# Kernel optimization log

Hardware: AMD Instinct MI355X
Metric: run time of the kernel (lower is better)

Reference implementation:

```python
import jax, jax.numpy as jnp
import numpy as np

B, T, D, H = 64, 512, 256, 512

def _xavier(key, shape):
    fan_in, fan_out = shape
    lim = np.sqrt(6.0 / (fan_in + fan_out))
    return jax.random.uniform(key, shape, jnp.float32, -lim, lim)

def setup_inputs() -> dict:
    key = jax.random.key(0)
    ks = jax.random.split(key, 16)
    inp = {
        'x': jax.random.normal(ks[0], (B, T, D), jnp.float32),
        'h': jax.random.normal(ks[1], (B, H), jnp.float32),
        'We2h': _xavier(ks[2], (D, H)),            # err_in2h (no bias)
        'Wr_x': _xavier(ks[3], (D, H)),
        'Wr_h': _xavier(ks[4], (H, H)),
        'Wr_e': _xavier(ks[5], (H, H)),
        'br': jnp.zeros((H,), jnp.float32),
        'Wz_x': _xavier(ks[6], (D, H)),
        'Wz_h': _xavier(ks[7], (H, H)),
        'Wz_e': _xavier(ks[8], (H, H)),
        'bz': jnp.ones((H,), jnp.float32),         # update_bias.fill_(1.0)
        'Wn_x': _xavier(ks[9], (D, H)),
        'Wn_h': _xavier(ks[10], (H, H)),
        'Wn_e': _xavier(ks[11], (H, H)),
        'bn': jnp.zeros((H,), jnp.float32),
        'Wo': _xavier(ks[12], (H, D)),             # readout Linear(H, D)
        'bo': jnp.zeros((D,), jnp.float32),
    }
    return inp

def reference(x, h, We2h, Wr_x, Wr_h, Wr_e, br, Wz_x, Wz_h, Wz_e, bz, Wn_x, Wn_h, Wn_e, bn, Wo, bo):
    # Precompute all input-to-hidden projections in large GEMMs: [B,T,H]
    x_e = jnp.einsum('btd,dh->bth', x, We2h)
    x_r = jnp.einsum('btd,dh->bth', x, Wr_x) + br
    x_z = jnp.einsum('btd,dh->bth', x, Wz_x) + bz
    x_n = jnp.einsum('btd,dh->bth', x, Wn_x) + bn
    # scan over time: inputs [T,B,H]
    xs = (jnp.swapaxes(x_e, 0, 1), jnp.swapaxes(x_r, 0, 1),
          jnp.swapaxes(x_z, 0, 1), jnp.swapaxes(x_n, 0, 1))

    def step(h, ins):
        xe_t, xr_t, xz_t, xn_t = ins
        e = xe_t - h                                   # innovation e_t
        r = jax.nn.sigmoid(xr_t + h @ Wr_h + e @ Wr_e)
        z = jax.nn.sigmoid(xz_t + h @ Wz_h + e @ Wz_e)
        n = jnp.tanh(xn_t + (r * h) @ Wn_h + (r * e) @ Wn_e)
        h_new = (1.0 - z) * h + z * n
        return h_new, h_new

    _, h_seq = jax.lax.scan(step, h, xs)               # [T,B,H]
    h_seq = jnp.swapaxes(h_seq, 0, 1)                  # [B,T,H]
    out = jnp.einsum('bth,hd->btd', h_seq, Wo) + bo    # [B,T,D]
    return out, h_seq
```

## Files before the change

### kernel.cpp

```cpp
#include <hip/hip_runtime.h>
#include <hip/hip_bf16.h>
#include <hip/hip_fp16.h>

#define B_ 64
#define T_ 512
#define D_ 256
#define H_ 512
#define M_ (B_*T_)

#define NBLK 64
#define JO 8

typedef unsigned int uint;
typedef __attribute__((ext_vector_type(8))) short bf16x8;
typedef __attribute__((ext_vector_type(4))) float f32x4;
typedef _Float16 half_t;
typedef __attribute__((ext_vector_type(2))) _Float16 half2_t;

__device__ __forceinline__ unsigned short f32_to_bf16(float f) {
    unsigned u = __builtin_bit_cast(unsigned, f);
    unsigned r = (u + 0x7fffu + ((u >> 16) & 1u)) >> 16;
    return (unsigned short)r;
}
__device__ __forceinline__ float bf16_to_f32(unsigned short h) {
    unsigned u = ((unsigned)h) << 16;
    return __builtin_bit_cast(float, u);
}
__device__ __forceinline__ unsigned pkh2(float a, float b) {
    half2_t h; h.x = (half_t)a; h.y = (half_t)b;
    return __builtin_bit_cast(unsigned, h);
}
__device__ __forceinline__ half2_t uph2(unsigned u) {
    return __builtin_bit_cast(half2_t, u);
}

#if __has_builtin(__builtin_amdgcn_fdot2)
__device__ __forceinline__ float fdot2(half2_t a, half2_t b, float c) {
    return __builtin_amdgcn_fdot2(a, b, c, false);
}
#else
__device__ __forceinline__ float fdot2(half2_t a, half2_t b, float c) {
    return c + (float)a.x * (float)b.x + (float)a.y * (float)b.y;
}
#endif

__device__ __forceinline__ uint ald(const uint* p) {
    return __hip_atomic_load(p, __ATOMIC_RELAXED, __HIP_MEMORY_SCOPE_AGENT);
}
__device__ __forceinline__ void ast(uint* p, uint v) {
    __hip_atomic_store(p, v, __ATOMIC_RELAXED, __HIP_MEMORY_SCOPE_AGENT);
}

__device__ __forceinline__ float sigmoidf_(float x) {
    return 1.f / (1.f + __expf(-x));
}

__device__ __forceinline__ void gbar(uint* flags, uint target, int tid, int bid) {
    __syncthreads();
    if (tid < 64) {
        if (tid == 0)
            __hip_atomic_store(&flags[bid * 4], target,
                               __ATOMIC_RELAXED, __HIP_MEMORY_SCOPE_AGENT);
        int it = 0;
        uint f;
        do {
            f = __hip_atomic_load(&flags[tid * 4],
                                  __ATOMIC_RELAXED, __HIP_MEMORY_SCOPE_AGENT);
            if (++it > (1 << 24)) break;
        } while (!__all(f >= target));
    }
    __builtin_amdgcn_s_barrier();
}

__global__ void comp_p(const float* __restrict__ We2h, const float* __restrict__ Wre,
                       const float* __restrict__ Wze,
                       float* __restrict__ Pr, float* __restrict__ Pz) {
    int tid = blockIdx.x * blockDim.x + threadIdx.x;
    if (tid >= 256 * 512) return;
    int k = tid >> 9, j = tid & 511;
    float ar = 0.f, az = 0.f;
    for (int kk = 0; kk < 512; kk++) {
        float e = We2h[k * 512 + kk];
        ar += e * Wre[kk * 512 + j];
        az += e * Wze[kk * 512 + j];
    }
    Pr[tid] = ar;
    Pz[tid] = az;
}

__global__ void build_wt(const float* __restrict__ We2h, const float* __restrict__ Wrx,
                         const float* __restrict__ Wzx, const float* __restrict__ Wnx,
                         const float* __restrict__ Pr, const float* __restrict__ Pz,
                         const float* __restrict__ br, const float* __restrict__ bz,
                         const float* __restrict__ bn, const float* __restrict__ Wo,
                         unsigned short* __restrict__ WcatT, float* __restrict__ biascat,
                         unsigned short* __restrict__ WoT) {
    int tid = blockIdx.x * blockDim.x + threadIdx.x;
    const int total1 = 2048 * 256;
    if (tid < total1) {
        int n = tid >> 8, k = tid & 255;
        int sel = n >> 9, nl = n & 511;
        float v;
        if (sel == 0)      v = We2h[k * 512 + nl];
        else if (sel == 1) v = Wrx[k * 512 + nl] + Pr[k * 512 + nl];
        else if (sel == 2) v = Wzx[k * 512 + nl] + Pz[k * 512 + nl];
        else               v = Wnx[k * 512 + nl];
        WcatT[tid] = f32_to_bf16(v);
        if (k == 0) {
            float bv = sel == 0 ? 0.f : sel == 1 ? br[nl] : sel == 2 ? bz[nl] : bn[nl];
            biascat[n] = bv;
        }
    } else {
        int t2 = tid - total1;
        if (t2 < 256 * 512) {
            int n = t2 >> 9, k = t2 & 511;
            WoT[t2] = f32_to_bf16(Wo[k * 256 + n]);
        }
    }
}

__global__ void build_wscan(const float* __restrict__ Wrh, const float* __restrict__ Wre,
                            const float* __restrict__ Wzh, const float* __restrict__ Wze,
                            const float* __restrict__ Wnh, const float* __restrict__ Wne,
                            uint2* __restrict__ warz, uint* __restrict__ wan) {
    int tid = blockIdx.x * blockDim.x + threadIdx.x;
    if (tid < 256 * 512) {
        int kp = tid >> 9, j = tid & 511;
        int k0 = 2 * kp;
        float ar0 = Wrh[k0 * 512 + j] - Wre[k0 * 512 + j];
        float ar1 = Wrh[(k0 + 1) * 512 + j] - Wre[(k0 + 1) * 512 + j];
        float az0 = Wzh[k0 * 512 + j] - Wze[k0 * 512 + j];
        float az1 = Wzh[(k0 + 1) * 512 + j] - Wze[(k0 + 1) * 512 + j];
        warz[tid] = make_uint2(pkh2(ar0, ar1), pkh2(az0, az1));
    }
    int t2 = tid - 256 * 512;
    if (t2 >= 0 && t2 < 512 * 512) {
        int k = t2 >> 9, j = t2 & 511;
        float an = Wnh[k * 512 + j] - Wne[k * 512 + j];
        wan[t2] = pkh2(an, Wne[k * 512 + j]);
    }
}

__global__ void init_hbuf(const float* __restrict__ h0, uint* __restrict__ hbuf) {
    int tid = blockIdx.x * blockDim.x + threadIdx.x;
    if (tid >= 256 * 64) return;
    int kp = tid >> 6, m = tid & 63;
    hbuf[tid] = pkh2(h0[m * 512 + 2 * kp], h0[m * 512 + 2 * kp + 1]);
}

__global__ __launch_bounds__(256)
void gemmx_kernel(const float* __restrict__ A, const unsigned short* __restrict__ BT,
                  const float* __restrict__ bias, unsigned short* __restrict__ xT) {
    __shared__ unsigned short Asm[128 * 64];
    __shared__ unsigned short Bsm[128 * 64];
    __shared__ unsigned short Csm[128][128];
    const int tid = threadIdx.x;
    const int t0 = blockIdx.x * 2;
    const int c0 = blockIdx.y * 128;
    const int lane = tid & 63, wid = tid >> 6;
    const int wm = wid >> 1, wn = wid & 1;
    const int lr = lane & 15, lg = lane >> 4;

    f32x4 acc[4][4] = {};

    const int srow = tid >> 1, shalf = tid & 1;
    const int rowA = (srow & 63) * 512 + t0 + (srow >> 6);
    const float* Arow = A + (size_t)rowA * 256 + shalf * 32;
    const unsigned short* Brow = BT + (size_t)(c0 + srow) * 256 + shalf * 32;
    unsigned short* As = &Asm[srow * 64 + shalf * 32];
    unsigned short* Bs = &Bsm[srow * 64 + shalf * 32];

    for (int kt = 0; kt < 256; kt += 64) {
#pragma unroll
        for (int q = 0; q < 8; q++) {
            float4 v = *(const float4*)(Arow + kt + q * 4);
            unsigned p0 = ((unsigned)f32_to_bf16(v.y) << 16) | f32_to_bf16(v.x);
            unsigned p1 = ((unsigned)f32_to_bf16(v.w) << 16) | f32_to_bf16(v.z);
            *(uint2*)(As + q * 4) = make_uint2(p0, p1);
        }
#pragma unroll
        for (int q = 0; q < 4; q++) {
            uint4 v = *(const uint4*)(Brow + kt + q * 8);
            *(uint4*)(Bs + q * 8) = v;
        }
        __syncthreads();
#pragma unroll
        for (int ks = 0; ks < 2; ks++) {
            bf16x8 af[4], bfr[4];
#pragma unroll
            for (int m = 0; m < 4; m++)
                af[m] = *(const bf16x8*)&Asm[(wm * 64 + m * 16 + lr) * 64 + ks * 32 + lg * 8];
#pragma unroll
            for (int n2 = 0; n2 < 4; n2++)
                bfr[n2] = *(const bf16x8*)&Bsm[(wn * 64 + n2 * 16 + lr) * 64 + ks * 32 + lg * 8];
#pragma unroll
            for (int m = 0; m < 4; m++)
#pragma unroll
                for (int n2 = 0; n2 < 4; n2++)
                    acc[m][n2] = __builtin_amdgcn_mfma_f32_16x16x32_bf16(
                        af[m], bfr[n2], acc[m][n2], 0, 0, 0);
        }
        __syncthreads();
    }
#pragma unroll
    for (int m = 0; m < 4; m++) {
        int r0 = wm * 64 + m * 16 + lg * 4;
#pragma unroll
        for (int n2 = 0; n2 < 4; n2++) {
            int c = wn * 64 + n2 * 16 + lr;
            float bv = bias[c0 + c];
#pragma unroll
            for (int i = 0; i < 4; i++)
                Csm[c][r0 + i] = f32_to_bf16(acc[m][n2][i] + bv);
        }
    }
    __syncthreads();
#pragma unroll
    for (int th = 0; th < 2; th++) {
        uint4* dst = (uint4*)(xT + ((size_t)(t0 + th) * 2048 + c0) * 64);
        for (int q = tid; q < 1024; q += 256) {
            int c = q >> 3, b0 = (q & 7) * 8;
            dst[q] = *(const uint4*)&Csm[c][th * 64 + b0];
        }
        __syncthreads();
    }
}

__global__ __launch_bounds__(256)
void gemm_out_kernel(const float* __restrict__ A, const unsigned short* __restrict__ BT,
                     const float* __restrict__ bias, float* __restrict__ C,
                     int M, int N, int K) {
    __shared__ unsigned short Asm[128 * 64];
    __shared__ unsigned short Bsm[128 * 64];
    const int tid = threadIdx.x;
    const int bm = blockIdx.x, bn = blockIdx.y;
    const int lane = tid & 63, wid = tid >> 6;
    const int wm = wid >> 1, wn = wid & 1;
    const int lr = lane & 15, lg = lane >> 4;

    f32x4 acc[4][4] = {};

    const int srow = tid >> 1, shalf = tid & 1;
    const float* Arow = A + (size_t)(bm * 128 + srow) * K + shalf * 32;
    const unsigned short* Brow = BT + (size_t)(bn * 128 + srow) * K + shalf * 32;
    unsigned short* As = &Asm[srow * 64 + shalf * 32];
    unsigned short* Bs = &Bsm[srow * 64 + shalf * 32];

    for (int kt = 0; kt < K; kt += 64) {
#pragma unroll
        for (int q = 0; q < 8; q++) {
            float4 v = *(const float4*)(Arow + kt + q * 4);
            unsigned p0 = ((unsigned)f32_to_bf16(v.y) << 16) | f32_to_bf16(v.x);
            unsigned p1 = ((unsigned)f32_to_bf16(v.w) << 16) | f32_to_bf16(v.z);
            *(uint2*)(As + q * 4) = make_uint2(p0, p1);
        }
#pragma unroll
        for (int q = 0; q < 4; q++) {
            uint4 v = *(const uint4*)(Brow + kt + q * 8);
            *(uint4*)(Bs + q * 8) = v;
        }
        __syncthreads();
#pragma unroll
        for (int ks = 0; ks < 2; ks++) {
            bf16x8 af[4], bfr[4];
#pragma unroll
            for (int m = 0; m < 4; m++)
                af[m] = *(const bf16x8*)&Asm[(wm * 64 + m * 16 + lr) * 64 + ks * 32 + lg * 8];
#pragma unroll
            for (int n2 = 0; n2 < 4; n2++)
                bfr[n2] = *(const bf16x8*)&Bsm[(wn * 64 + n2 * 16 + lr) * 64 + ks * 32 + lg * 8];
#pragma unroll
            for (int m = 0; m < 4; m++)
#pragma unroll
                for (int n2 = 0; n2 < 4; n2++)
                    acc[m][n2] = __builtin_amdgcn_mfma_f32_16x16x32_bf16(
                        af[m], bfr[n2], acc[m][n2], 0, 0, 0);
        }
        __syncthreads();
    }
#pragma unroll
    for (int m = 0; m < 4; m++) {
        int row0 = bm * 128 + wm * 64 + m * 16 + lg * 4;
#pragma unroll
        for (int n2 = 0; n2 < 4; n2++) {
            int col = bn * 128 + wn * 64 + n2 * 16 + lr;
            float bv = bias[col];
#pragma unroll
            for (int i = 0; i < 4; i++)
                C[(size_t)(row0 + i) * N + col] = acc[m][n2][i] + bv;
        }
    }
}

__global__ __launch_bounds__(512)
void scan_sync(const unsigned short* __restrict__ xT,
               const float* __restrict__ h0,
               const uint2* __restrict__ warz,
               const uint* __restrict__ wan,
               uint* __restrict__ hbuf,
               uint* __restrict__ rhrxe,
               uint* __restrict__ flags,
               float* __restrict__ hseq)
{
    __shared__ uint2 Wrz_l[256][JO];
    __shared__ uint  Wn_l[512][JO];
    __shared__ float part[3][8][JO][64];
    __shared__ float h_loc[JO][64], z_loc[JO][64];

    const int bid = blockIdx.x, tid = threadIdx.x;
    const int lane = tid & 63, wv = tid >> 6;
    const int j0 = bid * JO;
    const int jF = tid >> 6, mF = tid & 63;

    for (int i = tid; i < 256 * JO; i += 512) {
        int kp = i >> 3, j = i & 7;
        Wrz_l[kp][j] = warz[kp * 512 + j0 + j];
    }
    for (int i = tid; i < 512 * JO; i += 512) {
        int k = i >> 3, j = i & 7;
        Wn_l[k][j] = wan[k * 512 + j0 + j];
    }
    h_loc[jF][mF] = h0[mF * 512 + j0 + jF];
    __syncthreads();

    const int jg = j0 + jF;
    const size_t xoff = (size_t)jg * 64 + mF;
    unsigned short pxe = xT[xoff];
    unsigned short pxr = xT[xoff + (size_t)512 * 64];
    unsigned short pxz = xT[xoff + (size_t)1024 * 64];
    unsigned short pxn = xT[xoff + (size_t)1536 * 64];

    for (int t = 0; t < T_; t++) {
        {
            uint hv[32];
#pragma unroll
            for (int q = 0; q < 32; q++)
                hv[q] = ald(&hbuf[(wv * 32 + q) * 64 + lane]);
            float ar[JO] = {}, az[JO] = {};
#pragma unroll
            for (int q = 0; q < 32; q++) {
                half2_t h2 = uph2(hv[q]);
#pragma unroll
                for (int j = 0; j < JO; j++) {
                    uint2 w = *(const uint2*)&Wrz_l[wv * 32 + q][j];
                    ar[j] = fdot2(h2, uph2(w.x), ar[j]);
                    az[j] = fdot2(h2, uph2(w.y), az[j]);
                }
            }
#pragma unroll
            for (int j = 0; j < JO; j++) {
                part[0][wv][j][lane] = ar[j];
                part[1][wv][j][lane] = az[j];
            }
        }
        __syncthreads();

        float xe = bf16_to_f32(pxe), xn_f = bf16_to_f32(pxn);
        {
            float sr = 0.f, sz = 0.f;
#pragma unroll
            for (int w = 0; w < 8; w++) { sr += part[0][w][jF][mF]; sz += part[1][w][jF][mF]; }
            float r = sigmoidf_(bf16_to_f32(pxr) + sr);
            float z = sigmoidf_(bf16_to_f32(pxz) + sz);
            float h = h_loc[jF][mF];
            z_loc[jF][mF] = z;
            ast(&rhrxe[jg * 64 + mF], pkh2(r * h, r * xe));
        }
        gbar(flags, 2u * (uint)t + 1u, tid, bid);

        {
            float an[JO] = {};
#pragma unroll
            for (int ch = 0; ch < 2; ch++) {
                uint rv[32];
#pragma unroll
                for (int q = 0; q < 32; q++)
                    rv[q] = ald(&rhrxe[(wv * 64 + ch * 32 + q) * 64 + lane]);
#pragma unroll
                for (int q = 0; q < 32; q++) {
                    half2_t p2 = uph2(rv[q]);
#pragma unroll
                    for (int j = 0; j < JO; j++)
                        an[j] = fdot2(p2, uph2(Wn_l[wv * 64 + ch * 32 + q][j]), an[j]);
                }
            }
#pragma unroll
            for (int j = 0; j < JO; j++) part[2][wv][j][lane] = an[j];
        }
        __syncthreads();

        {
            float sn = 0.f;
#pragma unroll
            for (int w = 0; w < 8; w++) sn += part[2][w][jF][mF];
            float nn = tanhf(xn_f + sn);
            float z = z_loc[jF][mF];
            float h = h_loc[jF][mF];
            h_loc[jF][mF] = (1.f - z) * h + z * nn;
        }
        __syncthreads();

        if (tid < (JO / 2) * 64) {
            int jp = tid >> 6, mh = tid & 63;
            ast(&hbuf[(bid * (JO / 2) + jp) * 64 + mh],
                pkh2(h_loc[2 * jp][mh], h_loc[2 * jp + 1][mh]));
        }
        {
            int js = tid & 7, ms = tid >> 3;
            hseq[((size_t)ms * 512 + t) * 512 + j0 + js] = h_loc[js][ms];
        }

        __syncthreads();
        if (t + 1 < T_) {
            const size_t xb = (size_t)(t + 1) * 2048 * 64 + xoff;
            pxe = xT[xb];
            pxr = xT[xb + (size_t)512 * 64];
            pxz = xT[xb + (size_t)1024 * 64];
            pxn = xT[xb + (size_t)1536 * 64];
        }
        __builtin_amdgcn_sched_barrier(0);
        if (tid < 64) {
            if (tid == 0)
                __hip_atomic_store(&flags[bid * 4], 2u * (uint)t + 2u,
                                   __ATOMIC_RELAXED, __HIP_MEMORY_SCOPE_AGENT);
            int it = 0;
            uint f;
            do {
                f = __hip_atomic_load(&flags[tid * 4],
                                      __ATOMIC_RELAXED, __HIP_MEMORY_SCOPE_AGENT);
                if (++it > (1 << 24)) break;
            } while (!__all(f >= 2u * (uint)t + 2u));
        }
        __builtin_amdgcn_s_barrier();
    }
}

extern "C" void kernel_launch(void* const* d_in, const int* in_sizes, int n_in,
                              void* d_out, int out_size, void* d_ws, size_t ws_size,
                              hipStream_t stream) {
    const float* x    = (const float*)d_in[0];
    const float* h0   = (const float*)d_in[1];
    const float* We2h = (const float*)d_in[2];
    const float* Wrx  = (const float*)d_in[3];
    const float* Wrh  = (const float*)d_in[4];
    const float* Wre  = (const float*)d_in[5];
    const float* br   = (const float*)d_in[6];
    const float* Wzx  = (const float*)d_in[7];
    const float* Wzh  = (const float*)d_in[8];
    const float* Wze  = (const float*)d_in[9];
    const float* bz   = (const float*)d_in[10];
    const float* Wnx  = (const float*)d_in[11];
    const float* Wnh  = (const float*)d_in[12];
    const float* Wne  = (const float*)d_in[13];
    const float* bn   = (const float*)d_in[14];
    const float* Wo   = (const float*)d_in[15];
    const float* bo   = (const float*)d_in[16];

    char* w = (char*)d_ws;
    unsigned short* xT    = (unsigned short*)(w);
    uint2*          warz  = (uint2*)(w + 134217728);
    uint*           wan   = (uint*)(w + 135266304);
    unsigned short* WcatT = (unsigned short*)(w + 136314880);
    unsigned short* WoT   = (unsigned short*)(w + 137363456);
    float*          biascat = (float*)(w + 137625600);
    float*          Pr    = (float*)(w + 137633792);
    float*          Pz    = (float*)(w + 138158080);
    uint*           hbuf  = (uint*)(w + 138682368);
    uint*           rhrxe = (uint*)(w + 138747904);
    uint*           flags = (uint*)(w + 138878976);

    float* out  = (float*)d_out;
    float* hseq = (float*)d_out + (size_t)M_ * D_;

    hipMemsetAsync(flags, 0, NBLK * 4 * sizeof(uint), stream);

    comp_p<<<(256 * 512 + 255) / 256, 256, 0, stream>>>(We2h, Wre, Wze, Pr, Pz);
    build_wt<<<(2048 * 256 + 256 * 512 + 255) / 256, 256, 0, stream>>>(
        We2h, Wrx, Wzx, Wnx, Pr, Pz, br, bz, bn, Wo, WcatT, biascat, WoT);
    build_wscan<<<(256 * 512 + 512 * 512 + 255) / 256, 256, 0, stream>>>(
        Wrh, Wre, Wzh, Wze, Wnh, Wne, warz, wan);
    init_hbuf<<<(256 * 64 + 255) / 256, 256, 0, stream>>>(h0, hbuf);

    {
        dim3 grid(T_ / 2, 2048 / 128);
        gemmx_kernel<<<grid, 256, 0, stream>>>(x, WcatT, biascat, xT);
    }
    scan_sync<<<NBLK, 512, 0, stream>>>(xT, h0, warz, wan, hbuf, rhrxe, flags, hseq);
    {
        dim3 grid(M_ / 128, D_ / 128);
        gemm_out_kernel<<<grid, 256, 0, stream>>>(hseq, WoT, bo, out, M_, D_, H_);
    }
}
```

Before: 5.560 ms.

## Split scan batch into two halves with per-half flags to overlap grid barriers

Splits the 64-wide batch of the recurrent scan into two 32-row halves, each with its own set of global progress flags. Blocks now wait only on the flags of the half they are about to consume. This lets work on one half overlap with other blocks still finishing the other half, instead of every block stalling at a full grid barrier. Each wave's reduction over k is split across the two 32-lane halves and combined with a lane shuffle. In exchange there are twice as many flag waits and block barriers per step, and the x-projection loads are no longer prefetched one step ahead.

Result: slower. 5.968 ms (+7.3%).

```diff
diff --git a/kernel.cpp b/kernel.cpp
--- a/kernel.cpp
+++ b/kernel.cpp
@@ -53,23 +53,6 @@
 
 __device__ __forceinline__ float sigmoidf_(float x) {
     return 1.f / (1.f + __expf(-x));
-}
-
-__device__ __forceinline__ void gbar(uint* flags, uint target, int tid, int bid) {
-    __syncthreads();
-    if (tid < 64) {
-        if (tid == 0)
-            __hip_atomic_store(&flags[bid * 4], target,
-                               __ATOMIC_RELAXED, __HIP_MEMORY_SCOPE_AGENT);
-        int it = 0;
-        uint f;
-        do {
-            f = __hip_atomic_load(&flags[tid * 4],
-                                  __ATOMIC_RELAXED, __HIP_MEMORY_SCOPE_AGENT);
-            if (++it > (1 << 24)) break;
-        } while (!__all(f >= target));
-    }
-    __builtin_amdgcn_s_barrier();
 }
 
 __global__ void comp_p(const float* __restrict__ We2h, const float* __restrict__ Wre,
@@ -304,13 +287,14 @@
 {
     __shared__ uint2 Wrz_l[256][JO];
     __shared__ uint  Wn_l[512][JO];
-    __shared__ float part[3][8][JO][64];
+    __shared__ float part[3][8][JO][32];
     __shared__ float h_loc[JO][64], z_loc[JO][64];
 
     const int bid = blockIdx.x, tid = threadIdx.x;
     const int lane = tid & 63, wv = tid >> 6;
     const int j0 = bid * JO;
     const int jF = tid >> 6, mF = tid & 63;
+    const int ml = lane & 31, kq = lane >> 5;
 
     for (int i = tid; i < 256 * JO; i += 512) {
         int kp = i >> 3, j = i & 7;
@@ -325,113 +309,126 @@
 
     const int jg = j0 + jF;
     const size_t xoff = (size_t)jg * 64 + mF;
-    unsigned short pxe = xT[xoff];
-    unsigned short pxr = xT[xoff + (size_t)512 * 64];
-    unsigned short pxz = xT[xoff + (size_t)1024 * 64];
-    unsigned short pxn = xT[xoff + (size_t)1536 * 64];
 
     for (int t = 0; t < T_; t++) {
-        {
-            uint hv[32];
-#pragma unroll
-            for (int q = 0; q < 32; q++)
-                hv[q] = ald(&hbuf[(wv * 32 + q) * 64 + lane]);
+        const size_t xb = (size_t)t * 2048 * 64 + xoff;
+        unsigned short pxe = xT[xb];
+        unsigned short pxr = xT[xb + (size_t)512 * 64];
+        unsigned short pxz = xT[xb + (size_t)1024 * 64];
+        unsigned short pxn = xT[xb + (size_t)1536 * 64];
+
+#pragma unroll
+        for (int mh = 0; mh < 2; mh++) {
+            if (tid < 64) {
+                int it = 0; uint f;
+                do {
+                    f = ald(&flags[(2 + mh) * 256 + tid * 4]);
+                    if (++it > (1 << 24)) break;
+                } while (!__all(f >= (uint)t));
+            }
+            __builtin_amdgcn_s_barrier();
+
+            uint hv[16];
+#pragma unroll
+            for (int q = 0; q < 16; q++)
+                hv[q] = ald(&hbuf[(wv * 32 + 2 * q + kq) * 64 + mh * 32 + ml]);
             float ar[JO] = {}, az[JO] = {};
 #pragma unroll
-            for (int q = 0; q < 32; q++) {
+            for (int q = 0; q < 16; q++) {
                 half2_t h2 = uph2(hv[q]);
+                const int kp = wv * 32 + 2 * q + kq;
 #pragma unroll
                 for (int j = 0; j < JO; j++) {
-                    uint2 w = *(const uint2*)&Wrz_l[wv * 32 + q][j];
+                    uint2 w = *(const uint2*)&Wrz_l[kp][j];
                     ar[j] = fdot2(h2, uph2(w.x), ar[j]);
                     az[j] = fdot2(h2, uph2(w.y), az[j]);
                 }
             }
 #pragma unroll
             for (int j = 0; j < JO; j++) {
-                part[0][wv][j][lane] = ar[j];
-                part[1][wv][j][lane] = az[j];
-            }
-        }
-        __syncthreads();
-
-        float xe = bf16_to_f32(pxe), xn_f = bf16_to_f32(pxn);
-        {
-            float sr = 0.f, sz = 0.f;
-#pragma unroll
-            for (int w = 0; w < 8; w++) { sr += part[0][w][jF][mF]; sz += part[1][w][jF][mF]; }
-            float r = sigmoidf_(bf16_to_f32(pxr) + sr);
-            float z = sigmoidf_(bf16_to_f32(pxz) + sz);
-            float h = h_loc[jF][mF];
-            z_loc[jF][mF] = z;
-            ast(&rhrxe[jg * 64 + mF], pkh2(r * h, r * xe));
-        }
-        gbar(flags, 2u * (uint)t + 1u, tid, bid);
-
-        {
+                ar[j] += __shfl_xor(ar[j], 32);
+                az[j] += __shfl_xor(az[j], 32);
+            }
+            if (lane < 32) {
+#pragma unroll
+                for (int j = 0; j < JO; j++) {
+                    part[0][wv][j][ml] = ar[j];
+                    part[1][wv][j][ml] = az[j];
+                }
+            }
+            __syncthreads();
+
+            if ((mF >> 5) == mh) {
+                float sr = 0.f, sz = 0.f;
+#pragma unroll
+                for (int w = 0; w < 8; w++) {
+                    sr += part[0][w][jF][mF & 31];
+                    sz += part[1][w][jF][mF & 31];
+                }
+                float r = sigmoidf_(bf16_to_f32(pxr) + sr);
+                float z = sigmoidf_(bf16_to_f32(pxz) + sz);
+                float h = h_loc[jF][mF];
+                z_loc[jF][mF] = z;
+                ast(&rhrxe[jg * 64 + mF], pkh2(r * h, r * bf16_to_f32(pxe)));
+            }
+            __syncthreads();
+            if (tid == 0) ast(&flags[mh * 256 + bid * 4], (uint)t + 1u);
+        }
+
+#pragma unroll
+        for (int mh = 0; mh < 2; mh++) {
+            if (tid < 64) {
+                int it = 0; uint f;
+                do {
+                    f = ald(&flags[mh * 256 + tid * 4]);
+                    if (++it > (1 << 24)) break;
+                } while (!__all(f >= (uint)t + 1u));
+            }
+            __builtin_amdgcn_s_barrier();
+
+            uint rv[32];
+#pragma unroll
+            for (int q = 0; q < 32; q++)
+                rv[q] = ald(&rhrxe[(wv * 64 + 2 * q + kq) * 64 + mh * 32 + ml]);
             float an[JO] = {};
 #pragma unroll
-            for (int ch = 0; ch < 2; ch++) {
-                uint rv[32];
-#pragma unroll
-                for (int q = 0; q < 32; q++)
-                    rv[q] = ald(&rhrxe[(wv * 64 + ch * 32 + q) * 64 + lane]);
-#pragma unroll
-                for (int q = 0; q < 32; q++) {
-                    half2_t p2 = uph2(rv[q]);
-#pragma unroll
-                    for (int j = 0; j < JO; j++)
-                        an[j] = fdot2(p2, uph2(Wn_l[wv * 64 + ch * 32 + q][j]), an[j]);
-                }
-            }
-#pragma unroll
-            for (int j = 0; j < JO; j++) part[2][wv][j][lane] = an[j];
-        }
-        __syncthreads();
-
-        {
-            float sn = 0.f;
-#pragma unroll
-            for (int w = 0; w < 8; w++) sn += part[2][w][jF][mF];
-            float nn = tanhf(xn_f + sn);
-            float z = z_loc[jF][mF];
-            float h = h_loc[jF][mF];
-            h_loc[jF][mF] = (1.f - z) * h + z * nn;
-        }
-        __syncthreads();
-
-        if (tid < (JO / 2) * 64) {
-            int jp = tid >> 6, mh = tid & 63;
-            ast(&hbuf[(bid * (JO / 2) + jp) * 64 + mh],
-                pkh2(h_loc[2 * jp][mh], h_loc[2 * jp + 1][mh]));
-        }
-        {
-            int js = tid & 7, ms = tid >> 3;
-            hseq[((size_t)ms * 512 + t) * 512 + j0 + js] = h_loc[js][ms];
-        }
-
-        __syncthreads();
-        if (t + 1 < T_) {
-            const size_t xb = (size_t)(t + 1) * 2048 * 64 + xoff;
-            pxe = xT[xb];
-            pxr = xT[xb + (size_t)512 * 64];
-            pxz = xT[xb + (size_t)1024 * 64];
-            pxn = xT[xb + (size_t)1536 * 64];
-        }
-        __builtin_amdgcn_sched_barrier(0);
-        if (tid < 64) {
-            if (tid == 0)
-                __hip_atomic_store(&flags[bid * 4], 2u * (uint)t + 2u,
-                                   __ATOMIC_RELAXED, __HIP_MEMORY_SCOPE_AGENT);
-            int it = 0;
-            uint f;
-            do {
-                f = __hip_atomic_load(&flags[tid * 4],
-                                      __ATOMIC_RELAXED, __HIP_MEMORY_SCOPE_AGENT);
-                if (++it > (1 << 24)) break;
-            } while (!__all(f >= 2u * (uint)t + 2u));
-        }
-        __builtin_amdgcn_s_barrier();
+            for (int q = 0; q < 32; q++) {
+                half2_t p2 = uph2(rv[q]);
+                const int k = wv * 64 + 2 * q + kq;
+#pragma unroll
+                for (int j = 0; j < JO; j++)
+                    an[j] = fdot2(p2, uph2(Wn_l[k][j]), an[j]);
+            }
+#pragma unroll
+            for (int j = 0; j < JO; j++) an[j] += __shfl_xor(an[j], 32);
+            if (lane < 32) {
+#pragma unroll
+                for (int j = 0; j < JO; j++) part[2][wv][j][ml] = an[j];
+            }
+            __syncthreads();
+
+            if ((mF >> 5) == mh) {
+                float sn = 0.f;
+#pragma unroll
+                for (int w = 0; w < 8; w++) sn += part[2][w][jF][mF & 31];
+                float nn = tanhf(bf16_to_f32(pxn) + sn);
+                float z = z_loc[jF][mF];
+                float h = h_loc[jF][mF];
+                h_loc[jF][mF] = (1.f - z) * h + z * nn;
+            }
+            __syncthreads();
+
+            if (((mF >> 5) == mh) && ((jF & 1) == 0))
+                ast(&hbuf[(bid * 4 + (jF >> 1)) * 64 + mF],
+                    pkh2(h_loc[jF][mF], h_loc[jF + 1][mF]));
+            {
+                int js = tid & 7, ms = tid >> 3;
+                if ((ms >> 5) == mh)
+                    hseq[((size_t)ms * 512 + t) * 512 + j0 + js] = h_loc[js][ms];
+            }
+            __syncthreads();
+            if (tid == 0) ast(&flags[(2 + mh) * 256 + bid * 4], (uint)t + 1u);
+        }
     }
 }
 
@@ -472,7 +469,7 @@
     float* out  = (float*)d_out;
     float* hseq = (float*)d_out + (size_t)M_ * D_;
 
-    hipMemsetAsync(flags, 0, NBLK * 4 * sizeof(uint), stream);
+    hipMemsetAsync(flags, 0, 4 * 256 * sizeof(uint), stream);
 
     comp_p<<<(256 * 512 + 255) / 256, 256, 0, stream>>>(We2h, Wre, Wze, Pr, Pz);
     build_wt<<<(2048 * 256 + 256 * 512 + 255) / 256, 256, 0, stream>>>(
```

## Replace grid barriers with per-wave producer flag waits in the GRU scan

Applied to the files above, without the earlier changes.

The full grid barriers in the recurrent scan are replaced by two flag arrays, one for the r·h/r·e exchange and one for the new hidden state. Each wave spins only on the eight producer blocks whose slices it actually reads, and the trailing end-of-step barrier is dropped. The aim is to cut cross-block synchronisation cost per timestep and let the hseq store overlap the next step. In exchange, the per-step xT loads are no longer prefetched a step ahead and now sit at the top of each iteration, so their latency is exposed unless the spin wait hides it.

Result: faster. 4.997 ms (-10.1%).

```diff
diff --git a/kernel.cpp b/kernel.cpp
--- a/kernel.cpp
+++ b/kernel.cpp
@@ -55,21 +55,9 @@
     return 1.f / (1.f + __expf(-x));
 }
 
-__device__ __forceinline__ void gbar(uint* flags, uint target, int tid, int bid) {
-    __syncthreads();
-    if (tid < 64) {
-        if (tid == 0)
-            __hip_atomic_store(&flags[bid * 4], target,
-                               __ATOMIC_RELAXED, __HIP_MEMORY_SCOPE_AGENT);
-        int it = 0;
-        uint f;
-        do {
-            f = __hip_atomic_load(&flags[tid * 4],
-                                  __ATOMIC_RELAXED, __HIP_MEMORY_SCOPE_AGENT);
-            if (++it > (1 << 24)) break;
-        } while (!__all(f >= target));
-    }
-    __builtin_amdgcn_s_barrier();
+__device__ __forceinline__ void spin_fence() {
+    asm volatile("" ::: "memory");
+    __builtin_amdgcn_sched_barrier(0);
 }
 
 __global__ void comp_p(const float* __restrict__ We2h, const float* __restrict__ Wre,
@@ -312,6 +300,9 @@
     const int j0 = bid * JO;
     const int jF = tid >> 6, mF = tid & 63;
 
+    uint* flagA = flags;
+    uint* flagH = flags + 256;
+
     for (int i = tid; i < 256 * JO; i += 512) {
         int kp = i >> 3, j = i & 7;
         Wrz_l[kp][j] = warz[kp * 512 + j0 + j];
@@ -325,12 +316,26 @@
 
     const int jg = j0 + jF;
     const size_t xoff = (size_t)jg * 64 + mF;
-    unsigned short pxe = xT[xoff];
-    unsigned short pxr = xT[xoff + (size_t)512 * 64];
-    unsigned short pxz = xT[xoff + (size_t)1024 * 64];
-    unsigned short pxn = xT[xoff + (size_t)1536 * 64];
+    const bool plane = (lane < 8);
+    uint* pA = plane ? &flagA[(8 * wv + lane) * 4] : (uint*)0;
+    uint* pH = plane ? &flagH[(8 * wv + lane) * 4] : (uint*)0;
 
     for (int t = 0; t < T_; t++) {
+        const size_t xb = (size_t)t * 2048 * 64 + xoff;
+        unsigned short pxe = xT[xb];
+        unsigned short pxr = xT[xb + (size_t)512 * 64];
+        unsigned short pxz = xT[xb + (size_t)1024 * 64];
+        unsigned short pxn = xT[xb + (size_t)1536 * 64];
+
+        {
+            int it = 0; uint f;
+            do {
+                f = plane ? ald(pH) : 0xFFFFFFFFu;
+                if (++it > (1 << 24)) break;
+            } while (!__all(f >= (uint)t));
+        }
+        spin_fence();
+
         {
             uint hv[32];
 #pragma unroll
@@ -366,7 +371,17 @@
             z_loc[jF][mF] = z;
             ast(&rhrxe[jg * 64 + mF], pkh2(r * h, r * xe));
         }
-        gbar(flags, 2u * (uint)t + 1u, tid, bid);
+        __syncthreads();
+        if (tid == 0) ast(&flagA[bid * 4], (uint)t + 1u);
+
+        {
+            int it = 0; uint f;
+            do {
+                f = plane ? ald(pA) : 0xFFFFFFFFu;
+                if (++it > (1 << 24)) break;
+            } while (!__all(f >= (uint)t + 1u));
+        }
+        spin_fence();
 
         {
             float an[JO] = {};
@@ -405,33 +420,13 @@
             ast(&hbuf[(bid * (JO / 2) + jp) * 64 + mh],
                 pkh2(h_loc[2 * jp][mh], h_loc[2 * jp + 1][mh]));
         }
+        __syncthreads();
+        if (tid == 0) ast(&flagH[bid * 4], (uint)t + 1u);
+
         {
             int js = tid & 7, ms = tid >> 3;
             hseq[((size_t)ms * 512 + t) * 512 + j0 + js] = h_loc[js][ms];
         }
-
-        __syncthreads();
-        if (t + 1 < T_) {
-            const size_t xb = (size_t)(t + 1) * 2048 * 64 + xoff;
-            pxe = xT[xb];
-            pxr = xT[xb + (size_t)512 * 64];
-            pxz = xT[xb + (size_t)1024 * 64];
-            pxn = xT[xb + (size_t)1536 * 64];
-        }
-        __builtin_amdgcn_sched_barrier(0);
-        if (tid < 64) {
-            if (tid == 0)
-                __hip_atomic_store(&flags[bid * 4], 2u * (uint)t + 2u,
-                                   __ATOMIC_RELAXED, __HIP_MEMORY_SCOPE_AGENT);
-            int it = 0;
-            uint f;
-            do {
-                f = __hip_atomic_load(&flags[tid * 4],
-                                      __ATOMIC_RELAXED, __HIP_MEMORY_SCOPE_AGENT);
-                if (++it > (1 << 24)) break;
-            } while (!__all(f >= 2u * (uint)t + 2u));
-        }
-        __builtin_amdgcn_s_barrier();
     }
 }
 
@@ -472,7 +467,7 @@
     float* out  = (float*)d_out;
     float* hseq = (float*)d_out + (size_t)M_ * D_;
 
-    hipMemsetAsync(flags, 0, NBLK * 4 * sizeof(uint), stream);
+    hipMemsetAsync(flags, 0, 2048, stream);
 
     comp_p<<<(256 * 512 + 255) / 256, 256, 0, stream>>>(We2h, Wre, Wze, Pr, Pz);
     build_wt<<<(2048 * 256 + 256 * 512 + 255) / 256, 256, 0, stream>>>(
```
